# Kernel optimization log

Hardware: AMD Instinct MI355X
Metric: run time of the kernel (lower is better)

The kernel has to match this reference:

```python
import jax, jax.numpy as jnp
import numpy as np

N, E, D = 50000, 1200000, 64
NEG_SLOPE = 0.2  # PyG GATConv LeakyReLU slope
EPS_SM = 1e-16   # PyG softmax eps
EPS_LN = 1e-5


def _glorot(key, shape):
    fan = shape[0]
    return jax.random.normal(key, shape, jnp.float32) / np.float32(np.sqrt(fan))


def setup_inputs() -> dict:
    key = jax.random.key(0)
    ks = jax.random.split(key, 16)
    inp = {
        "x": jax.random.normal(ks[0], (N, D), jnp.float32),
        "edge_index": jax.random.randint(ks[1], (2, E), 0, N, dtype=jnp.int32),
        # layer 0: bipartite-style (-1,-1) GATConv -> separate src/dst projections
        "W_src0": _glorot(ks[2], (D, D)), "W_dst0": _glorot(ks[3], (D, D)),
        "a_src0": _glorot(ks[4], (D,)), "a_dst0": _glorot(ks[5], (D,)),
        "b0": jnp.zeros((D,), jnp.float32),
        "lin_W0": _glorot(ks[6], (D, D)), "lin_b0": jnp.zeros((D,), jnp.float32),
        # layers 1,2: int in_channels -> shared projection for src and dst
        "W1": _glorot(ks[7], (D, D)),
        "a_src1": _glorot(ks[8], (D,)), "a_dst1": _glorot(ks[9], (D,)),
        "b1": jnp.zeros((D,), jnp.float32),
        "lin_W1": _glorot(ks[10], (D, D)), "lin_b1": jnp.zeros((D,), jnp.float32),
        "W2": _glorot(ks[11], (D, D)),
        "a_src2": _glorot(ks[12], (D,)), "a_dst2": _glorot(ks[13], (D,)),
        "b2": jnp.zeros((D,), jnp.float32),
        "lin_W2": _glorot(ks[14], (D, D)), "lin_b2": jnp.zeros((D,), jnp.float32),
        "ln_w": jnp.ones((D,), jnp.float32), "ln_b": jnp.zeros((D,), jnp.float32),
        "proj_W": _glorot(ks[15], (D, 1)), "proj_b": jnp.zeros((1,), jnp.float32),
    }
    return inp


def _gat(x_src, x_dst, a_src, a_dst, bias, src, dst):
    # per-edge attention logit: a_src.x_j + a_dst.x_i, LeakyReLU
    alpha = (x_src * a_src).sum(-1)[src] + (x_dst * a_dst).sum(-1)[dst]  # [E]
    alpha = jnp.where(alpha >= 0, alpha, NEG_SLOPE * alpha)
    # segment softmax over edges sharing a destination node
    m = jax.ops.segment_max(alpha, dst, num_segments=N)
    m = jnp.where(jnp.isfinite(m), m, 0.0)  # empty segments -> -inf -> 0
    e = jnp.exp(alpha - m[dst])
    denom = jax.ops.segment_sum(e, dst, num_segments=N)
    w = e / (denom[dst] + EPS_SM)
    # weighted scatter-add aggregation
    return jax.ops.segment_sum(w[:, None] * x_src[src], dst, num_segments=N) + bias


def reference(x, edge_index,
              W_src0, W_dst0, a_src0, a_dst0, b0, lin_W0, lin_b0,
              W1, a_src1, a_dst1, b1, lin_W1, lin_b1,
              W2, a_src2, a_dst2, b2, lin_W2, lin_b2,
              ln_w, ln_b, proj_W, proj_b):
    src, dst = edge_index[0], edge_index[1]
    h = _gat(x @ W_src0, x @ W_dst0, a_src0, a_dst0, b0, src, dst) + x @ lin_W0 + lin_b0
    h = jax.nn.relu(h)
    hp = h @ W1
    h = _gat(hp, hp, a_src1, a_dst1, b1, src, dst) + h @ lin_W1 + lin_b1
    h = jax.nn.relu(h)
    hp = h @ W2
    h = _gat(hp, hp, a_src2, a_dst2, b2, src, dst) + h @ lin_W2 + lin_b2
    # PyG LayerNorm mode='graph': normalize over all nodes and channels
    mu = h.mean()
    var = h.var()
    h = (h - mu) * jax.lax.rsqrt(var + EPS_LN) * ln_w + ln_b
    return h @ proj_W + proj_b  # [N, 1]
```

## Files before the change

kernel.cpp:

```cpp
#include <hip/hip_runtime.h>
#include <hip/hip_bf16.h>

#define NN 50000
#define NE 1200000
#define D 64
#define NEG_SLOPE 0.2f
#define EPS_SM 1e-16f
#define EPS_LN 1e-5f
#define KMAX 4
#define BSH 6
#define NBUK 782
#define BCAP 2048
#define BCAPSH 11
#define EPB 4096
#define NPB 293
#define GP_NODES 32
#define GP_BLOCKS 1563
#define GAT_BLOCKS 12500

__device__ __forceinline__ float waveReduceSum(float v) {
    #pragma unroll
    for (int off = 32; off > 0; off >>= 1)
        v += __shfl_xor(v, off, 64);
    return v;
}
__device__ __forceinline__ float waveReduceMax(float v) {
    #pragma unroll
    for (int off = 32; off > 0; off >>= 1)
        v = fmaxf(v, __shfl_xor(v, off, 64));
    return v;
}

template <bool HASD>
__global__ __launch_bounds__(256) void gemm_proj(
                          const float* __restrict__ hin,
                          const float* __restrict__ Wsrc,
                          const float* __restrict__ Wdst,
                          const float* __restrict__ Wlin,
                          const float* __restrict__ avs,
                          const float* __restrict__ avd,
                          const float* __restrict__ bgat,
                          const float* __restrict__ blin,
                          __hip_bfloat16* __restrict__ hp,
                          float* __restrict__ agg,
                          float* __restrict__ alpha_s,
                          float* __restrict__ alpha_d) {
    __shared__ float xt[GP_NODES * D];
    const int t   = threadIdx.x;
    const int nb0 = blockIdx.x * GP_NODES;
    const float4* src4 = (const float4*)(hin + (size_t)nb0 * D);
    float4* dst4 = (float4*)xt;
    if (nb0 + GP_NODES <= NN) {
        dst4[t]       = src4[t];
        dst4[t + 256] = src4[t + 256];
    } else {
        #pragma unroll
        for (int i = 0; i < 2; ++i) {
            const int idx = t + 256 * i;
            const int node = nb0 + (idx >> 4);
            dst4[idx] = (node < NN) ? src4[idx] : make_float4(0.f, 0.f, 0.f, 0.f);
        }
    }
    __syncthreads();

    const int wv   = t >> 6;
    const int lane = t & 63;
    const float* xw = xt + wv * 8 * D;

    float accs[8], accl[8], accd[HASD ? 8 : 1];
    #pragma unroll
    for (int m = 0; m < 8; ++m) { accs[m] = 0.f; accl[m] = 0.f; }
    if (HASD) {
        #pragma unroll
        for (int m = 0; m < 8; ++m) accd[m] = 0.f;
    }

    #pragma unroll 4
    for (int k = 0; k < D; k += 4) {
        float ws[4], wl[4], wd[4];
        #pragma unroll
        for (int j = 0; j < 4; ++j) {
            ws[j] = Wsrc[(k + j) * D + lane];
            wl[j] = Wlin[(k + j) * D + lane];
            if (HASD) wd[j] = Wdst[(k + j) * D + lane];
        }
        #pragma unroll
        for (int m = 0; m < 8; ++m) {
            const float4 xm = *(const float4*)(xw + m * D + k);
            accs[m] = fmaf(xm.x, ws[0], accs[m]);
            accs[m] = fmaf(xm.y, ws[1], accs[m]);
            accs[m] = fmaf(xm.z, ws[2], accs[m]);
            accs[m] = fmaf(xm.w, ws[3], accs[m]);
            accl[m] = fmaf(xm.x, wl[0], accl[m]);
            accl[m] = fmaf(xm.y, wl[1], accl[m]);
            accl[m] = fmaf(xm.z, wl[2], accl[m]);
            accl[m] = fmaf(xm.w, wl[3], accl[m]);
            if (HASD) {
                accd[m] = fmaf(xm.x, wd[0], accd[m]);
                accd[m] = fmaf(xm.y, wd[1], accd[m]);
                accd[m] = fmaf(xm.z, wd[2], accd[m]);
                accd[m] = fmaf(xm.w, wd[3], accd[m]);
            }
        }
    }

    const float avs_l = avs[lane], avd_l = avd[lane];
    const float bias  = blin[lane] + bgat[lane];
    #pragma unroll
    for (int m = 0; m < 8; ++m) {
        const int node = nb0 + wv * 8 + m;
        const float vs = waveReduceSum(accs[m] * avs_l);
        const float vd = waveReduceSum((HASD ? accd[m] : accs[m]) * avd_l);
        if (node < NN) {
            hp[(size_t)node * D + lane]  = __float2bfloat16(accs[m]);
            agg[(size_t)node * D + lane] = accl[m] + bias;
            if (lane == 0) {
                alpha_s[node] = vs;
                alpha_d[node] = vd;
            }
        }
    }
}

__global__ void zero_ints(int* __restrict__ p, int n) {
    const int i = blockIdx.x * blockDim.x + threadIdx.x;
    if (i < n) p[i] = 0;
}

__global__ __launch_bounds__(256) void bucket_partition(const int* __restrict__ ei,
                                                        int* __restrict__ bcur,
                                                        int2* __restrict__ pairs) {
    __shared__ int h[NBUK];
    __shared__ int cur[NBUK];
    for (int i = threadIdx.x; i < NBUK; i += 256) h[i] = 0;
    __syncthreads();
    const int base = blockIdx.x * EPB;
    const int lim  = min(EPB, NE - base);
    for (int i = threadIdx.x; i < lim; i += 256)
        atomicAdd(&h[ei[NE + base + i] >> BSH], 1);
    __syncthreads();
    for (int i = threadIdx.x; i < NBUK; i += 256) {
        const int c = h[i];
        cur[i] = c ? atomicAdd(&bcur[i], c) : 0;
    }
    __syncthreads();
    for (int i = threadIdx.x; i < lim; i += 256) {
        const int s = ei[base + i];
        const int d = ei[NE + base + i];
        const int b = d >> BSH;
        const int pos = atomicAdd(&cur[b], 1);
        if (pos < BCAP) pairs[(b << BCAPSH) + pos] = make_int2(s, d);
    }
}

__global__ __launch_bounds__(256) void csr_finalize(const int2* __restrict__ pairs,
                                                    const int* __restrict__ bcur,
                                                    int* __restrict__ cnt,
                                                    int* __restrict__ row_start,
                                                    int* __restrict__ csr_src) {
    __shared__ int ncnt[64];
    __shared__ int lsrc[BCAP];
    const int t = threadIdx.x;
    const int b = blockIdx.x;
    const int beg = b << BCAPSH;
    const int m = min(bcur[b], BCAP);
    const int nbase = b << BSH;
    if (t < 64) ncnt[t] = 0;
    __syncthreads();
    for (int i = t; i < m; i += 256)
        atomicAdd(&ncnt[pairs[beg + i].y - nbase], 1);
    __syncthreads();
    if (t < 64) {
        const int v = ncnt[t];
        int inc = v;
        #pragma unroll
        for (int off = 1; off < 64; off <<= 1) {
            const int u = __shfl_up(inc, off, 64);
            if (t >= off) inc += u;
        }
        const int excl = inc - v;
        if (nbase + t < NN) {
            cnt[nbase + t] = v;
            row_start[nbase + t] = beg + excl;
        }
        ncnt[t] = excl;
    }
    __syncthreads();
    for (int i = t; i < m; i += 256) {
        const int2 p = pairs[beg + i];
        const int pos = atomicAdd(&ncnt[p.y - nbase], 1);
        lsrc[pos] = p.x;
    }
    __syncthreads();
    for (int i = t; i < m; i += 256)
        csr_src[beg + i] = lsrc[i];
}

template <bool DO_RELU, bool DO_STATS>
__global__ __launch_bounds__(256) void gat_node(
                         const int* __restrict__ csr_src,
                         const int* __restrict__ row_start,
                         const int* __restrict__ cnt,
                         const float* __restrict__ as,
                         const float* __restrict__ ad,
                         const __hip_bfloat16* __restrict__ hp,
                         float* __restrict__ agg,
                         float* __restrict__ partial) {
    __shared__ int2 esm[4][KMAX * 64];
    const int wv   = threadIdx.x >> 6;
    const int lane = threadIdx.x & 63;
    const int node = blockIdx.x * 4 + wv;
    const int snode = __builtin_amdgcn_readfirstlane(node);
    const int deg = cnt[snode];
    const int rs  = row_start[snode];
    const int half = lane >> 5;
    const int c2   = lane & 31;
    float2 acc = make_float2(0.f, 0.f);
    if (deg > 0) {
        const float ad_d = ad[snode];
        int   sr[KMAX];
        float ea[KMAX];
        float mx = -INFINITY;
        #pragma unroll
        for (int k = 0; k < KMAX; ++k) {
            const int j = k * 64 + lane;
            const bool valid = j < deg;
            const int s = valid ? csr_src[rs + j] : 0;
            float a = valid ? (as[s] + ad_d) : -INFINITY;
            a = (a >= 0.f) ? a : NEG_SLOPE * a;
            sr[k] = s;
            ea[k] = a;
            mx = fmaxf(mx, a);
        }
        mx = waveReduceMax(mx);
        float sum = 0.f;
        #pragma unroll
        for (int k = 0; k < KMAX; ++k) {
            float e = __expf(ea[k] - mx);
            e = (k * 64 + lane < deg) ? e : 0.f;
            ea[k] = e;
            sum += e;
        }
        sum = waveReduceSum(sum);
        const float inv = 1.f / (sum + EPS_SM);
        #pragma unroll
        for (int k = 0; k < KMAX; ++k) {
            if (k * 64 < deg)
                esm[wv][k * 64 + lane] = make_int2(sr[k] * 32, __float_as_int(ea[k] * inv));
        }
        const unsigned* hp32 = (const unsigned*)hp;
        const int jmax = (deg + 1) & ~1;
        float2 a0 = make_float2(0.f, 0.f), a1 = make_float2(0.f, 0.f);
        int j = 0;
        for (; j + 8 <= jmax; j += 8) {
            const int2 p0 = esm[wv][j + 0 + half];
            const int2 p1 = esm[wv][j + 2 + half];
            const int2 p2 = esm[wv][j + 4 + half];
            const int2 p3 = esm[wv][j + 6 + half];
            const unsigned v0 = hp32[p0.x + c2];
            const unsigned v1 = hp32[p1.x + c2];
            const unsigned v2 = hp32[p2.x + c2];
            const unsigned v3 = hp32[p3.x + c2];
            const float w0 = __int_as_float(p0.y), w1 = __int_as_float(p1.y);
            const float w2 = __int_as_float(p2.y), w3 = __int_as_float(p3.y);
            a0.x = fmaf(w0, __uint_as_float(v0 << 16), a0.x);
            a0.y = fmaf(w0, __uint_as_float(v0 & 0xffff0000u), a0.y);
            a1.x = fmaf(w1, __uint_as_float(v1 << 16), a1.x);
            a1.y = fmaf(w1, __uint_as_float(v1 & 0xffff0000u), a1.y);
            a0.x = fmaf(w2, __uint_as_float(v2 << 16), a0.x);
            a0.y = fmaf(w2, __uint_as_float(v2 & 0xffff0000u), a0.y);
            a1.x = fmaf(w3, __uint_as_float(v3 << 16), a1.x);
            a1.y = fmaf(w3, __uint_as_float(v3 & 0xffff0000u), a1.y);
        }
        for (; j < jmax; j += 2) {
            const int2 p = esm[wv][j + half];
            const unsigned v = hp32[p.x + c2];
            const float w = __int_as_float(p.y);
            a0.x = fmaf(w, __uint_as_float(v << 16), a0.x);
            a0.y = fmaf(w, __uint_as_float(v & 0xffff0000u), a0.y);
        }
        acc.x = a0.x + a1.x;
        acc.y = a0.y + a1.y;
    }
    acc.x += __shfl_xor(acc.x, 32, 64);
    acc.y += __shfl_xor(acc.y, 32, 64);

    float2 r2 = make_float2(0.f, 0.f);
    if (half == 0) {
        const float2 g = *(const float2*)(agg + (size_t)node * D + 2 * c2);
        r2.x = g.x + acc.x;
        r2.y = g.y + acc.y;
        if (DO_RELU) { r2.x = fmaxf(r2.x, 0.f); r2.y = fmaxf(r2.y, 0.f); }
        *(float2*)(agg + (size_t)node * D + 2 * c2) = r2;
    }
    if (DO_STATS) {
        float s  = r2.x + r2.y;
        float ss = r2.x * r2.x + r2.y * r2.y;
        s  = waveReduceSum(s);
        ss = waveReduceSum(ss);
        __shared__ float red[2][4];
        if (lane == 0) { red[0][wv] = s; red[1][wv] = ss; }
        __syncthreads();
        if (threadIdx.x == 0) {
            partial[blockIdx.x]              = red[0][0] + red[0][1] + red[0][2] + red[0][3];
            partial[GAT_BLOCKS + blockIdx.x] = red[1][0] + red[1][1] + red[1][2] + red[1][3];
        }
    }
}

__global__ void ln_reduce(const float* __restrict__ partial, float* __restrict__ stats) {
    float s = 0.f, ss = 0.f;
    for (int i = threadIdx.x; i < GAT_BLOCKS; i += 256) {
        s  += partial[i];
        ss += partial[GAT_BLOCKS + i];
    }
    s  = waveReduceSum(s);
    ss = waveReduceSum(ss);
    __shared__ float sm[2][4];
    if ((threadIdx.x & 63) == 0) {
        sm[0][threadIdx.x >> 6] = s;
        sm[1][threadIdx.x >> 6] = ss;
    }
    __syncthreads();
    if (threadIdx.x == 0) {
        stats[0] = sm[0][0] + sm[0][1] + sm[0][2] + sm[0][3];
        stats[1] = sm[1][0] + sm[1][1] + sm[1][2] + sm[1][3];
    }
}

__global__ void finalize(const float* __restrict__ x,
                         const float* __restrict__ stats,
                         const float* __restrict__ lnw,
                         const float* __restrict__ lnb,
                         const float* __restrict__ pw,
                         const float* __restrict__ pb,
                         float* __restrict__ out) {
    const int wave = (blockIdx.x * blockDim.x + threadIdx.x) >> 6;
    const int lane = threadIdx.x & 63;
    if (wave >= NN) return;
    const float inv_nd = 1.f / (float)(NN * D);
    const float mu  = stats[0] * inv_nd;
    const float var = stats[1] * inv_nd - mu * mu;
    const float rs = rsqrtf(var + EPS_LN);
    const float v = x[(size_t)wave * D + lane];
    const float xn = (v - mu) * rs * lnw[lane] + lnb[lane];
    const float c = waveReduceSum(xn * pw[lane]);
    if (lane == 0) out[wave] = c + pb[0];
}

extern "C" void kernel_launch(void* const* d_in, const int* in_sizes, int n_in,
                              void* d_out, int out_size, void* d_ws, size_t ws_size,
                              hipStream_t stream) {
    const float* x     = (const float*)d_in[0];
    const int*   ei    = (const int*)d_in[1];
    const float* Wsrc0 = (const float*)d_in[2];
    const float* Wdst0 = (const float*)d_in[3];
    const float* asrc0 = (const float*)d_in[4];
    const float* adst0 = (const float*)d_in[5];
    const float* b0    = (const float*)d_in[6];
    const float* linW0 = (const float*)d_in[7];
    const float* linb0 = (const float*)d_in[8];
    const float* W1    = (const float*)d_in[9];
    const float* asrc1 = (const float*)d_in[10];
    const float* adst1 = (const float*)d_in[11];
    const float* b1    = (const float*)d_in[12];
    const float* linW1 = (const float*)d_in[13];
    const float* linb1 = (const float*)d_in[14];
    const float* W2    = (const float*)d_in[15];
    const float* asrc2 = (const float*)d_in[16];
    const float* adst2 = (const float*)d_in[17];
    const float* b2    = (const float*)d_in[18];
    const float* linW2 = (const float*)d_in[19];
    const float* linb2 = (const float*)d_in[20];
    const float* lnw   = (const float*)d_in[21];
    const float* lnb   = (const float*)d_in[22];
    const float* pW    = (const float*)d_in[23];
    const float* pb    = (const float*)d_in[24];
    float* out = (float*)d_out;

    int*  csr_src   = (int*)d_ws;
    int*  cnt       = csr_src + NBUK * BCAP;
    int*  row_start = cnt + NN;
    int*  bcur      = row_start + NN;
    size_t off = (size_t)(NBUK * BCAP + 2 * NN + NBUK);
    off = (off + 3) & ~(size_t)3;
    float* A     = (float*)d_ws + off;
    int2*  pairs = (int2*)A;
    float* B     = A + (size_t)NBUK * BCAP * 2;
    __hip_bfloat16* P = (__hip_bfloat16*)(B + NN * D);
    float* alpha_s = (float*)(P + NN * D);
    float* alpha_d = alpha_s + NN;
    float* stats   = alpha_d + NN;
    float* partial = stats + 2;

    const int elem_blocks = (NN * D) / 256;

    zero_ints<<<(NBUK + 255) / 256, 256, 0, stream>>>(bcur, NBUK);
    bucket_partition<<<NPB, 256, 0, stream>>>(ei, bcur, pairs);
    csr_finalize<<<NBUK, 256, 0, stream>>>(pairs, bcur, cnt, row_start, csr_src);

    gemm_proj<true><<<GP_BLOCKS, 256, 0, stream>>>(x, Wsrc0, Wdst0, linW0, asrc0, adst0,
                                                   b0, linb0, P, A, alpha_s, alpha_d);
    gat_node<true, false><<<GAT_BLOCKS, 256, 0, stream>>>(csr_src, row_start, cnt,
                                                          alpha_s, alpha_d, P, A, partial);

    gemm_proj<false><<<GP_BLOCKS, 256, 0, stream>>>(A, W1, W1, linW1, asrc1, adst1,
                                                    b1, linb1, P, B, alpha_s, alpha_d);
    gat_node<true, false><<<GAT_BLOCKS, 256, 0, stream>>>(csr_src, row_start, cnt,
                                                          alpha_s, alpha_d, P, B, partial);

    gemm_proj<false><<<GP_BLOCKS, 256, 0, stream>>>(B, W2, W2, linW2, asrc2, adst2,
                                                    b2, linb2, P, A, alpha_s, alpha_d);
    gat_node<false, true><<<GAT_BLOCKS, 256, 0, stream>>>(csr_src, row_start, cnt,
                                                          alpha_s, alpha_d, P, A, partial);

    ln_reduce<<<1, 256, 0, stream>>>(partial, stats);
    finalize<<<elem_blocks, 256, 0, stream>>>(A, stats, lnw, lnb, pW, pb, out);
}
```

Baseline: 365.9 us.

## Split GAT aggregation into two channel-half passes with stored softmax weights

Splits each GAT aggregation kernel into two launches. The first computes the softmax weights, stores them to a new workspace buffer and aggregates channels 0-31. The second reloads those weights and aggregates channels 32-63. Each wave now handles 4 edges at a time with 16 lanes per edge, which halves the gathered row footprint per pass and is meant to improve cache hit rate on the bf16 feature gathers. Several loads and stores become nontemporal. The cost is an extra launch per layer plus extra traffic for writing and rereading the weights and CSR indices, and the LN partials now sum over both passes.

```diff
diff --git a/kernel.cpp b/kernel.cpp
--- a/kernel.cpp
+++ b/kernel.cpp
@@ -30,6 +30,8 @@
         v = fmaxf(v, __shfl_xor(v, off, 64));
     return v;
 }
+__device__ __forceinline__ float bflo(unsigned v) { return __uint_as_float(v << 16); }
+__device__ __forceinline__ float bfhi(unsigned v) { return __uint_as_float(v & 0xffff0000u); }
 
 template <bool HASD>
 __global__ __launch_bounds__(256) void gemm_proj(
@@ -197,7 +199,7 @@
 }
 
 template <bool DO_RELU, bool DO_STATS>
-__global__ __launch_bounds__(256) void gat_node(
+__global__ __launch_bounds__(256) void gat_half_lo(
                          const int* __restrict__ csr_src,
                          const int* __restrict__ row_start,
                          const int* __restrict__ cnt,
@@ -205,6 +207,7 @@
                          const float* __restrict__ ad,
                          const __hip_bfloat16* __restrict__ hp,
                          float* __restrict__ agg,
+                         float* __restrict__ wbuf,
                          float* __restrict__ partial) {
     __shared__ int2 esm[4][KMAX * 64];
     const int wv   = threadIdx.x >> 6;
@@ -213,8 +216,8 @@
     const int snode = __builtin_amdgcn_readfirstlane(node);
     const int deg = cnt[snode];
     const int rs  = row_start[snode];
-    const int half = lane >> 5;
-    const int c2   = lane & 31;
+    const int quad = lane >> 4;
+    const int c    = lane & 15;
     float2 acc = make_float2(0.f, 0.f);
     if (deg > 0) {
         const float ad_d = ad[snode];
@@ -225,7 +228,7 @@
         for (int k = 0; k < KMAX; ++k) {
             const int j = k * 64 + lane;
             const bool valid = j < deg;
-            const int s = valid ? csr_src[rs + j] : 0;
+            const int s = valid ? __builtin_nontemporal_load(csr_src + rs + j) : 0;
             float a = valid ? (as[s] + ad_d) : -INFINITY;
             a = (a >= 0.f) ? a : NEG_SLOPE * a;
             sr[k] = s;
@@ -245,53 +248,53 @@
         const float inv = 1.f / (sum + EPS_SM);
         #pragma unroll
         for (int k = 0; k < KMAX; ++k) {
-            if (k * 64 < deg)
-                esm[wv][k * 64 + lane] = make_int2(sr[k] * 32, __float_as_int(ea[k] * inv));
+            if (k * 64 < deg) {
+                const int j = k * 64 + lane;
+                const float w = ea[k] * inv;
+                if (j < deg) __builtin_nontemporal_store(w, wbuf + rs + j);
+                esm[wv][j] = make_int2(sr[k] * 32, __float_as_int(w));
+            }
         }
         const unsigned* hp32 = (const unsigned*)hp;
-        const int jmax = (deg + 1) & ~1;
+        const int jmax = (deg + 3) & ~3;
         float2 a0 = make_float2(0.f, 0.f), a1 = make_float2(0.f, 0.f);
         int j = 0;
         for (; j + 8 <= jmax; j += 8) {
-            const int2 p0 = esm[wv][j + 0 + half];
-            const int2 p1 = esm[wv][j + 2 + half];
-            const int2 p2 = esm[wv][j + 4 + half];
-            const int2 p3 = esm[wv][j + 6 + half];
-            const unsigned v0 = hp32[p0.x + c2];
-            const unsigned v1 = hp32[p1.x + c2];
-            const unsigned v2 = hp32[p2.x + c2];
-            const unsigned v3 = hp32[p3.x + c2];
+            const int2 p0 = esm[wv][j + quad];
+            const int2 p1 = esm[wv][j + 4 + quad];
+            const unsigned v0 = hp32[p0.x + c];
+            const unsigned v1 = hp32[p1.x + c];
             const float w0 = __int_as_float(p0.y), w1 = __int_as_float(p1.y);
-            const float w2 = __int_as_float(p2.y), w3 = __int_as_float(p3.y);
-            a0.x = fmaf(w0, __uint_as_float(v0 << 16), a0.x);
-            a0.y = fmaf(w0, __uint_as_float(v0 & 0xffff0000u), a0.y);
-            a1.x = fmaf(w1, __uint_as_float(v1 << 16), a1.x);
-            a1.y = fmaf(w1, __uint_as_float(v1 & 0xffff0000u), a1.y);
-            a0.x = fmaf(w2, __uint_as_float(v2 << 16), a0.x);
-            a0.y = fmaf(w2, __uint_as_float(v2 & 0xffff0000u), a0.y);
-            a1.x = fmaf(w3, __uint_as_float(v3 << 16), a1.x);
-            a1.y = fmaf(w3, __uint_as_float(v3 & 0xffff0000u), a1.y);
-        }
-        for (; j < jmax; j += 2) {
-            const int2 p = esm[wv][j + half];
-            const unsigned v = hp32[p.x + c2];
+            a0.x = fmaf(w0, bflo(v0), a0.x);
+            a0.y = fmaf(w0, bfhi(v0), a0.y);
+            a1.x = fmaf(w1, bflo(v1), a1.x);
+            a1.y = fmaf(w1, bfhi(v1), a1.y);
+        }
+        for (; j < jmax; j += 4) {
+            const int2 p = esm[wv][j + quad];
+            const unsigned v = hp32[p.x + c];
             const float w = __int_as_float(p.y);
-            a0.x = fmaf(w, __uint_as_float(v << 16), a0.x);
-            a0.y = fmaf(w, __uint_as_float(v & 0xffff0000u), a0.y);
+            a0.x = fmaf(w, bflo(v), a0.x);
+            a0.y = fmaf(w, bfhi(v), a0.y);
         }
         acc.x = a0.x + a1.x;
         acc.y = a0.y + a1.y;
     }
+    acc.x += __shfl_xor(acc.x, 16, 64);
+    acc.y += __shfl_xor(acc.y, 16, 64);
     acc.x += __shfl_xor(acc.x, 32, 64);
     acc.y += __shfl_xor(acc.y, 32, 64);
 
     float2 r2 = make_float2(0.f, 0.f);
-    if (half == 0) {
-        const float2 g = *(const float2*)(agg + (size_t)node * D + 2 * c2);
-        r2.x = g.x + acc.x;
-        r2.y = g.y + acc.y;
+    if (quad == 0) {
+        unsigned long long g = __builtin_nontemporal_load(
+            (const unsigned long long*)(agg + (size_t)node * D + 2 * c));
+        r2.x = __uint_as_float((unsigned)g) + acc.x;
+        r2.y = __uint_as_float((unsigned)(g >> 32)) + acc.y;
         if (DO_RELU) { r2.x = fmaxf(r2.x, 0.f); r2.y = fmaxf(r2.y, 0.f); }
-        *(float2*)(agg + (size_t)node * D + 2 * c2) = r2;
+        const unsigned long long o = (unsigned long long)__float_as_uint(r2.x) |
+                                     ((unsigned long long)__float_as_uint(r2.y) << 32);
+        __builtin_nontemporal_store(o, (unsigned long long*)(agg + (size_t)node * D + 2 * c));
     }
     if (DO_STATS) {
         float s  = r2.x + r2.y;
@@ -308,11 +311,97 @@
     }
 }
 
+template <bool DO_RELU, bool DO_STATS>
+__global__ __launch_bounds__(256) void gat_half_hi(
+                         const int* __restrict__ csr_src,
+                         const int* __restrict__ row_start,
+                         const int* __restrict__ cnt,
+                         const float* __restrict__ wbuf,
+                         const __hip_bfloat16* __restrict__ hp,
+                         float* __restrict__ agg,
+                         float* __restrict__ partial) {
+    __shared__ int2 esm[4][KMAX * 64];
+    const int wv   = threadIdx.x >> 6;
+    const int lane = threadIdx.x & 63;
+    const int node = blockIdx.x * 4 + wv;
+    const int snode = __builtin_amdgcn_readfirstlane(node);
+    const int deg = cnt[snode];
+    const int rs  = row_start[snode];
+    const int quad = lane >> 4;
+    const int c    = lane & 15;
+    float2 acc = make_float2(0.f, 0.f);
+    if (deg > 0) {
+        #pragma unroll
+        for (int k = 0; k < KMAX; ++k) {
+            if (k * 64 < deg) {
+                const int j = k * 64 + lane;
+                const bool valid = j < deg;
+                const int   s = valid ? __builtin_nontemporal_load(csr_src + rs + j) : 0;
+                const float w = valid ? __builtin_nontemporal_load(wbuf + rs + j) : 0.f;
+                esm[wv][j] = make_int2(s * 32, __float_as_int(w));
+            }
+        }
+        const unsigned* hp32 = (const unsigned*)hp;
+        const int jmax = (deg + 3) & ~3;
+        float2 a0 = make_float2(0.f, 0.f), a1 = make_float2(0.f, 0.f);
+        int j = 0;
+        for (; j + 8 <= jmax; j += 8) {
+            const int2 p0 = esm[wv][j + quad];
+            const int2 p1 = esm[wv][j + 4 + quad];
+            const unsigned v0 = hp32[p0.x + 16 + c];
+            const unsigned v1 = hp32[p1.x + 16 + c];
+            const float w0 = __int_as_float(p0.y), w1 = __int_as_float(p1.y);
+            a0.x = fmaf(w0, bflo(v0), a0.x);
+            a0.y = fmaf(w0, bfhi(v0), a0.y);
+            a1.x = fmaf(w1, bflo(v1), a1.x);
+            a1.y = fmaf(w1, bfhi(v1), a1.y);
+        }
+        for (; j < jmax; j += 4) {
+            const int2 p = esm[wv][j + quad];
+            const unsigned v = hp32[p.x + 16 + c];
+            const float w = __int_as_float(p.y);
+            a0.x = fmaf(w, bflo(v), a0.x);
+            a0.y = fmaf(w, bfhi(v), a0.y);
+        }
+        acc.x = a0.x + a1.x;
+        acc.y = a0.y + a1.y;
+    }
+    acc.x += __shfl_xor(acc.x, 16, 64);
+    acc.y += __shfl_xor(acc.y, 16, 64);
+    acc.x += __shfl_xor(acc.x, 32, 64);
+    acc.y += __shfl_xor(acc.y, 32, 64);
+
+    float2 r2 = make_float2(0.f, 0.f);
+    if (quad == 0) {
+        unsigned long long g = __builtin_nontemporal_load(
+            (const unsigned long long*)(agg + (size_t)node * D + 32 + 2 * c));
+        r2.x = __uint_as_float((unsigned)g) + acc.x;
+        r2.y = __uint_as_float((unsigned)(g >> 32)) + acc.y;
+        if (DO_RELU) { r2.x = fmaxf(r2.x, 0.f); r2.y = fmaxf(r2.y, 0.f); }
+        const unsigned long long o = (unsigned long long)__float_as_uint(r2.x) |
+                                     ((unsigned long long)__float_as_uint(r2.y) << 32);
+        __builtin_nontemporal_store(o, (unsigned long long*)(agg + (size_t)node * D + 32 + 2 * c));
+    }
+    if (DO_STATS) {
+        float s  = r2.x + r2.y;
+        float ss = r2.x * r2.x + r2.y * r2.y;
+        s  = waveReduceSum(s);
+        ss = waveReduceSum(ss);
+        __shared__ float red[2][4];
+        if (lane == 0) { red[0][wv] = s; red[1][wv] = ss; }
+        __syncthreads();
+        if (threadIdx.x == 0) {
+            partial[blockIdx.x]              = red[0][0] + red[0][1] + red[0][2] + red[0][3];
+            partial[GAT_BLOCKS + blockIdx.x] = red[1][0] + red[1][1] + red[1][2] + red[1][3];
+        }
+    }
+}
+
 __global__ void ln_reduce(const float* __restrict__ partial, float* __restrict__ stats) {
     float s = 0.f, ss = 0.f;
     for (int i = threadIdx.x; i < GAT_BLOCKS; i += 256) {
-        s  += partial[i];
-        ss += partial[GAT_BLOCKS + i];
+        s  += partial[i] + partial[2 * GAT_BLOCKS + i];
+        ss += partial[GAT_BLOCKS + i] + partial[3 * GAT_BLOCKS + i];
     }
     s  = waveReduceSum(s);
     ss = waveReduceSum(ss);
@@ -378,11 +467,12 @@
     const float* pb    = (const float*)d_in[24];
     float* out = (float*)d_out;
 
-    int*  csr_src   = (int*)d_ws;
-    int*  cnt       = csr_src + NBUK * BCAP;
-    int*  row_start = cnt + NN;
-    int*  bcur      = row_start + NN;
-    size_t off = (size_t)(NBUK * BCAP + 2 * NN + NBUK);
+    int*   csr_src   = (int*)d_ws;
+    float* wbuf      = (float*)(csr_src + NBUK * BCAP);
+    int*   cnt       = (int*)(wbuf + NBUK * BCAP);
+    int*   row_start = cnt + NN;
+    int*   bcur      = row_start + NN;
+    size_t off = (size_t)(2 * NBUK * BCAP + 2 * NN + NBUK);
     off = (off + 3) & ~(size_t)3;
     float* A     = (float*)d_ws + off;
     int2*  pairs = (int2*)A;
@@ -401,18 +491,24 @@
 
     gemm_proj<true><<<GP_BLOCKS, 256, 0, stream>>>(x, Wsrc0, Wdst0, linW0, asrc0, adst0,
                                                    b0, linb0, P, A, alpha_s, alpha_d);
-    gat_node<true, false><<<GAT_BLOCKS, 256, 0, stream>>>(csr_src, row_start, cnt,
-                                                          alpha_s, alpha_d, P, A, partial);
+    gat_half_lo<true, false><<<GAT_BLOCKS, 256, 0, stream>>>(csr_src, row_start, cnt,
+                                                  alpha_s, alpha_d, P, A, wbuf, partial);
+    gat_half_hi<true, false><<<GAT_BLOCKS, 256, 0, stream>>>(csr_src, row_start, cnt,
+                                                  wbuf, P, A, partial + 2 * GAT_BLOCKS);
 
     gemm_proj<false><<<GP_BLOCKS, 256, 0, stream>>>(A, W1, W1, linW1, asrc1, adst1,
                                                     b1, linb1, P, B, alpha_s, alpha_d);
-    gat_node<true, false><<<GAT_BLOCKS, 256, 0, stream>>>(csr_src, row_start, cnt,
-                                                          alpha_s, alpha_d, P, B, partial);
+    gat_half_lo<true, false><<<GAT_BLOCKS, 256, 0, stream>>>(csr_src, row_start, cnt,
+                                                  alpha_s, alpha_d, P, B, wbuf, partial);
+    gat_half_hi<true, false><<<GAT_BLOCKS, 256, 0, stream>>>(csr_src, row_start, cnt,
+                                                  wbuf, P, B, partial + 2 * GAT_BLOCKS);
 
     gemm_proj<false><<<GP_BLOCKS, 256, 0, stream>>>(B, W2, W2, linW2, asrc2, adst2,
                                                     b2, linb2, P, A, alpha_s, alpha_d);
-    gat_node<false, true><<<GAT_BLOCKS, 256, 0, stream>>>(csr_src, row_start, cnt,
-                                                          alpha_s, alpha_d, P, A, partial);
+    gat_half_lo<false, true><<<GAT_BLOCKS, 256, 0, stream>>>(csr_src, row_start, cnt,
+                                                  alpha_s, alpha_d, P, A, wbuf, partial);
+    gat_half_hi<false, true><<<GAT_BLOCKS, 256, 0, stream>>>(csr_src, row_start, cnt,
+                                                  wbuf, P, A, partial + 2 * GAT_BLOCKS);
 
     ln_reduce<<<1, 256, 0, stream>>>(partial, stats);
     finalize<<<elem_blocks, 256, 0, stream>>>(A, stats, lnw, lnb, pW, pb, out);
```

Measured after the change: 440.9 us. 20.5% more time.
